# Optimization experiments

Measured on AMD Instinct MI355X. Metric: run time of the kernel, lower is better.

## Reference

```python
import jax, jax.numpy as jnp
import numpy as np

B, L, D, F = 1, 4096, 4096, 11008
# (start, end, side): side 0 = vision expert, side 1 = language expert.
# Mirrors merge_section_size over alternating contiguous vision/language token ranges.
SEGMENTS = [(0, 1024, 0), (1024, 2048, 1), (2048, 3072, 0), (3072, 4096, 1)]


def setup_inputs() -> dict:
    key = jax.random.key(0)
    ks = jax.random.split(key, 7)
    s = 0.02  # weight init scale
    hidden_states = jax.random.normal(ks[0], (B, L, D), jnp.float32)
    tt = np.zeros((B, L), np.int32)
    for a, b, side in SEGMENTS:
        tt[:, a:b] = side
    token_type_ids = jnp.asarray(tt)
    lg_w = jax.random.normal(ks[1], (D, F), jnp.float32) * s
    lu_w = jax.random.normal(ks[2], (D, F), jnp.float32) * s
    ld_w = jax.random.normal(ks[3], (F, D), jnp.float32) * s
    vg_w = jax.random.normal(ks[4], (D, F), jnp.float32) * s
    vu_w = jax.random.normal(ks[5], (D, F), jnp.float32) * s
    vd_w = jax.random.normal(ks[6], (F, D), jnp.float32) * s
    return {
        'hidden_states': hidden_states,
        'token_type_ids': token_type_ids,
        'lg_w': lg_w, 'lu_w': lu_w, 'ld_w': ld_w,
        'vg_w': vg_w, 'vu_w': vu_w, 'vd_w': vd_w,
    }


def _swiglu_mlp(x, gw, uw, dw):
    # x: [B, T, D] -> [B, T, D]; down(silu(gate(x)) * up(x))
    h = jax.nn.silu(jnp.einsum('btd,df->btf', x, gw)) * jnp.einsum('btd,df->btf', x, uw)
    return jnp.einsum('btf,fd->btd', h, dw)


def reference(hidden_states, token_type_ids, lg_w, lu_w, ld_w, vg_w, vu_w, vd_w):
    # Split-dispatch over static contiguous segments, then concat along seq dim.
    outs = []
    for a, b, side in SEGMENTS:
        seg = hidden_states[:, a:b, :]
        if side == 1:
            outs.append(_swiglu_mlp(seg, lg_w, lu_w, ld_w))
        else:
            outs.append(_swiglu_mlp(seg, vg_w, vu_w, vd_w))
    return jnp.concatenate(outs, axis=1)
```

## Files before the change

### kernel.cpp

```cpp
#include <hip/hip_runtime.h>
#include <math.h>

typedef unsigned short u16;
typedef short s16x8 __attribute__((ext_vector_type(8)));
typedef float f32x16 __attribute__((ext_vector_type(16)));

#define GLOAD16(gp, lp)                                                        \
  __builtin_amdgcn_global_load_lds(                                            \
      (const __attribute__((address_space(1))) void*)(gp),                     \
      (__attribute__((address_space(3))) void*)(lp), 16, 0, 0)

__device__ __forceinline__ u16 f2bf(float f) {
  union { float f; unsigned u; } v; v.f = f;
  unsigned r = v.u + 0x7fffu + ((v.u >> 16) & 1u);
  return (u16)(r >> 16);
}

__global__ __launch_bounds__(256) void cvt_x_kernel(const float* __restrict__ in,
                                                    u16* __restrict__ out) {
  size_t i = ((size_t)blockIdx.x * 256 + threadIdx.x) * 8;
  float4 a = *(const float4*)(in + i);
  float4 b = *(const float4*)(in + i + 4);
  s16x8 v;
  v[0] = (short)f2bf(a.x); v[1] = (short)f2bf(a.y);
  v[2] = (short)f2bf(a.z); v[3] = (short)f2bf(a.w);
  v[4] = (short)f2bf(b.x); v[5] = (short)f2bf(b.y);
  v[6] = (short)f2bf(b.z); v[7] = (short)f2bf(b.w);
  *(s16x8*)(out + i) = v;
}

__global__ __launch_bounds__(256) void transpose_cvt_kernel(
    const float* __restrict__ in0, const float* __restrict__ in1,
    const float* __restrict__ in2, const float* __restrict__ in3,
    const float* __restrict__ in4, const float* __restrict__ in5,
    u16* __restrict__ o01, u16* __restrict__ o23,
    u16* __restrict__ o4, u16* __restrict__ o5) {
  __shared__ float s[64 * 65];
  const int mat = blockIdx.y;
  const float* in; u16* out;
  switch (mat) {
    case 0: in = in0; out = o01; break;
    case 1: in = in1; out = o01; break;
    case 2: in = in2; out = o23; break;
    case 3: in = in3; out = o23; break;
    case 4: in = in4; out = o4; break;
    default: in = in5; out = o5; break;
  }
  const int R = (mat < 4) ? 4096 : 11008;
  const int C = (mat < 4) ? 11008 : 4096;
  const int nTc = C >> 6;
  const int tr = blockIdx.x / nTc, tc = blockIdx.x - tr * nTc;
  const int r0 = tr << 6, c0 = tc << 6;
  const int t = threadIdx.x;
#pragma unroll
  for (int p = 0; p < 4; ++p) {
    const int lr = p * 16 + (t >> 4);
    const int lc = (t & 15) * 4;
    float4 v = *(const float4*)(in + (size_t)(r0 + lr) * C + (c0 + lc));
    float* sp = &s[lr * 65 + lc];
    sp[0] = v.x; sp[1] = v.y; sp[2] = v.z; sp[3] = v.w;
  }
  __syncthreads();
#pragma unroll
  for (int q = 0; q < 2; ++q) {
    const int oc = q * 32 + (t >> 3);
    const int orr = (t & 7) * 8;
    s16x8 v;
#pragma unroll
    for (int i = 0; i < 8; ++i) v[i] = (short)f2bf(s[(orr + i) * 65 + oc]);
    const int f = c0 + oc;
    size_t orow;
    if (mat < 4) orow = (size_t)((f >> 7) << 8) + ((mat & 1) << 7) + (f & 127);
    else         orow = (size_t)f;
    *(s16x8*)(out + orow * R + (r0 + orr)) = v;
  }
}

#define SBAR() __builtin_amdgcn_s_barrier()
#define LGKM0() asm volatile("s_waitcnt lgkmcnt(0)")
#define VMCNT6() asm volatile("s_waitcnt vmcnt(6)")
#define VMCNT0() asm volatile("s_waitcnt vmcnt(0)")

#define LDA(d, mh)                                                             \
  do {                                                                         \
    _Pragma("unroll") for (int fj = 0; fj < 2; ++fj)                           \
        _Pragma("unroll") for (int ks = 0; ks < 4; ++ks)                       \
        af[fj][ks] = *(const s16x8*)(ldsA + (d) * 32768 + (mh) * 16384 +       \
                                     arow + fj * 4096 + cx[ks]);               \
  } while (0)
#define LDB(d, nh)                                                             \
  do {                                                                         \
    _Pragma("unroll") for (int ks = 0; ks < 4; ++ks)                           \
        bf[nh][ks] = *(const s16x8*)(ldsB + (d) * 32768 + (nh) * 16384 +       \
                                     brow + cx[ks]);                           \
  } while (0)
#define MFMA8(mh, nh)                                                          \
  do {                                                                         \
    __builtin_amdgcn_s_setprio(1);                                             \
    _Pragma("unroll") for (int fj = 0; fj < 2; ++fj)                           \
        _Pragma("unroll") for (int ks = 0; ks < 4; ++ks)                       \
        acc[mh][fj][nh] = __builtin_amdgcn_mfma_f32_32x32x16_bf16(             \
            af[fj][ks], bf[nh][ks], acc[mh][fj][nh], 0, 0, 0);                 \
    __builtin_amdgcn_s_setprio(0);                                             \
  } while (0)

#define GEMM_PIPE3(FKv, HOOK)                                                  \
  do {                                                                         \
    STG_A(0, 0, 0); STG_B(0, 0, 0); STG_B(0, 1, 0); STG_A(0, 1, 0);            \
    STG_A(1, 0, 1); STG_B(1, 0, 1); STG_B(1, 1, 1);                            \
    VMCNT6(); SBAR();                                                          \
    for (int T = 0; T < (FKv)-2; ++T) {                                        \
      const int d = T & 1, nd = d ^ 1;                                         \
      LDA(d, 0); LDB(d, 0);                                                    \
      STG_A(nd, 1, T + 1);                                                     \
      LGKM0(); MFMA8(0, 0); SBAR();                                            \
      LDB(d, 1);                                                               \
      STG_A(d, 0, T + 2); STG_B(d, 0, T + 2);                                  \
      LGKM0(); MFMA8(0, 1); SBAR();                                            \
      LDA(d, 1);                                                               \
      STG_B(d, 1, T + 2);                                                      \
      LGKM0(); MFMA8(1, 1); MFMA8(1, 0);                                       \
      VMCNT6(); SBAR();                                                        \
      HOOK;                                                                    \
    }                                                                          \
    LDA(0, 0); LDB(0, 0);                                                      \
    STG_A(1, 1, (FKv)-1);                                                      \
    LGKM0(); MFMA8(0, 0); SBAR();                                              \
    LDB(0, 1);                                                                 \
    LGKM0(); MFMA8(0, 1); SBAR();                                              \
    LDA(0, 1);                                                                 \
    LGKM0(); MFMA8(1, 1); MFMA8(1, 0);                                         \
    VMCNT0(); SBAR();                                                          \
    LDA(1, 0); LDB(1, 0);                                                      \
    LGKM0(); MFMA8(0, 0); SBAR();                                              \
    LDB(1, 1);                                                                 \
    LGKM0(); MFMA8(0, 1); SBAR();                                              \
    LDA(1, 1);                                                                 \
    LGKM0(); MFMA8(1, 1); MFMA8(1, 0);                                         \
  } while (0)

#define ZERO_ACC()                                                             \
  do {                                                                         \
    _Pragma("unroll") for (int a = 0; a < 2; ++a)                              \
        _Pragma("unroll") for (int b = 0; b < 2; ++b)                          \
        _Pragma("unroll") for (int c2 = 0; c2 < 2; ++c2)                       \
        _Pragma("unroll") for (int r = 0; r < 16; ++r) acc[a][b][c2][r] = 0.f; \
  } while (0)

__global__ __launch_bounds__(512, 1) void gemm_gateup_persist(
    const u16* __restrict__ A, const u16* __restrict__ GUl,
    const u16* __restrict__ GUv, const int* __restrict__ tt,
    u16* __restrict__ H) {
  __shared__ u16 sA[2][2][128][64];
  __shared__ u16 sB[2][2][128][64];

  const int bid = blockIdx.x;
  const int c = ((bid >> 7) << 3) | (bid & 7);
  const int mT = (bid >> 3) & 15;
  const int ntiles = (c < 6) ? 6 : 5;
  const int FK = ntiles * 64;

  const int t = threadIdx.x;
  const int lane = t & 63;
  const int l31 = lane & 31;
  const int kg = lane >> 5;
  const int wn = (t >> 6) & 3;
  const int wm = (t >> 8) & 1;

  const int side = tt[mT << 8];
  const u16* GU = side ? GUl : GUv;

  const int rowq = t >> 3;
  const int gsw = ((t & 7) ^ (rowq & 7) ^ ((rowq >> 3) & 3)) << 4;
  const char* srcA = (const char*)A + (size_t)(mT * 256 + rowq) * 8192 + gsw;
  const char* srcB0 = (const char*)GU + ((size_t)(c * 256) + rowq) * 8192 + gsw;
  char* ldsA = (char*)&sA[0][0][0][0];
  char* ldsB = (char*)&sB[0][0][0][0];
  const int woff = (t & 448) << 4;

#define STG_A(d, h, q)                                                         \
  do {                                                                         \
    const char* _pa = srcA + ((q)&63) * 128;                                   \
    GLOAD16(_pa + (size_t)((h)*128) * 8192,                                    \
            ldsA + (d)*32768 + (h)*16384 + woff);                              \
    GLOAD16(_pa + (size_t)((h)*128 + 64) * 8192,                               \
            ldsA + (d)*32768 + (h)*16384 + 8192 + woff);                       \
  } while (0)
#define STG_B(d, h, q)                                                         \
  do {                                                                         \
    const char* _pb = srcB0 + (size_t)((q) >> 6) * 33554432 +                  \
                      (size_t)((h)*128) * 8192 + ((q)&63) * 128;               \
    GLOAD16(_pb, ldsB + (d)*32768 + (h)*16384 + woff);                         \
    GLOAD16(_pb + (size_t)64 * 8192,                                           \
            ldsB + (d)*32768 + (h)*16384 + 8192 + woff);                       \
  } while (0)

  const int arow = (wm * 64 + l31) * 128;
  const int brow = (wn * 32 + l31) * 128;
  int cx[4];
#pragma unroll
  for (int ks = 0; ks < 4; ++ks)
    cx[ks] = ((2 * ks + kg) ^ (l31 & 7) ^ ((l31 >> 3) & 3)) << 4;

  s16x8 af[2][4], bf[2][4];
  f32x16 acc[2][2][2];
  ZERO_ACC();

#define GU_EPI(nTv)                                                            \
  do {                                                                         \
    const int _nT = (nTv);                                                     \
    const int f = _nT * 128 + wn * 32 + l31;                                   \
    _Pragma("unroll") for (int mh = 0; mh < 2; ++mh)                           \
        _Pragma("unroll") for (int fj = 0; fj < 2; ++fj) {                     \
      const int rowbase = mT * 256 + mh * 128 + wm * 64 + fj * 32 + 4 * kg;    \
      _Pragma("unroll") for (int r = 0; r < 16; ++r) {                         \
        const int row = rowbase + (r & 3) + 8 * (r >> 2);                      \
        const float gv = acc[mh][fj][0][r];                                    \
        const float uv = acc[mh][fj][1][r];                                    \
        const float hv = gv / (1.f + __expf(-gv)) * uv;                        \
        H[(size_t)row * 11008 + f] = f2bf(hv);                                 \
      }                                                                        \
    }                                                                          \
  } while (0)

  GEMM_PIPE3(FK, if ((T & 63) == 63) { GU_EPI(c + 16 * (T >> 6)); ZERO_ACC(); });
  GU_EPI(c + 16 * (ntiles - 1));
#undef STG_A
#undef STG_B
#undef GU_EPI
}

__global__ __launch_bounds__(512, 1) void gemm_down(
    const u16* __restrict__ Hm, const u16* __restrict__ Dl,
    const u16* __restrict__ Dv, const int* __restrict__ tt,
    float* __restrict__ O) {
  constexpr int KB = 22016;
  __shared__ u16 sA[2][2][128][64];
  __shared__ u16 sB[2][2][128][64];

  const int bid = blockIdx.x;
  const int wg = (bid & 7) * 32 + (bid >> 3);
  const int mT = wg & 15;
  const int nT = wg >> 4;

  const int t = threadIdx.x;
  const int lane = t & 63;
  const int l31 = lane & 31;
  const int kg = lane >> 5;
  const int wn = (t >> 6) & 3;
  const int wm = (t >> 8) & 1;

  const int side = tt[mT << 8];
  const u16* B = side ? Dl : Dv;

  const int rowq = t >> 3;
  const int gsw = ((t & 7) ^ (rowq & 7) ^ ((rowq >> 3) & 3)) << 4;
  const char* srcA = (const char*)Hm + (size_t)(mT * 256 + rowq) * KB + gsw;
  const char* srcB = (const char*)B + (size_t)(nT * 256 + rowq) * KB + gsw;
  char* ldsA = (char*)&sA[0][0][0][0];
  char* ldsB = (char*)&sB[0][0][0][0];
  const int woff = (t & 448) << 4;

#define STG_A(d, h, q)                                                         \
  do {                                                                         \
    GLOAD16(srcA + (size_t)((h)*128) * KB + (size_t)(q)*128,                   \
            ldsA + (d)*32768 + (h)*16384 + woff);                              \
    GLOAD16(srcA + (size_t)((h)*128 + 64) * KB + (size_t)(q)*128,              \
            ldsA + (d)*32768 + (h)*16384 + 8192 + woff);                       \
  } while (0)
#define STG_B(d, h, q)                                                         \
  do {                                                                         \
    GLOAD16(srcB + (size_t)((h)*128) * KB + (size_t)(q)*128,                   \
            ldsB + (d)*32768 + (h)*16384 + woff);                              \
    GLOAD16(srcB + (size_t)((h)*128 + 64) * KB + (size_t)(q)*128,              \
            ldsB + (d)*32768 + (h)*16384 + 8192 + woff);                       \
  } while (0)

  const int arow = (wm * 64 + l31) * 128;
  const int brow = (wn * 32 + l31) * 128;
  int cx[4];
#pragma unroll
  for (int ks = 0; ks < 4; ++ks)
    cx[ks] = ((2 * ks + kg) ^ (l31 & 7) ^ ((l31 >> 3) & 3)) << 4;

  s16x8 af[2][4], bf[2][4];
  f32x16 acc[2][2][2];
  ZERO_ACC();

  GEMM_PIPE3(172, ;);

#pragma unroll
  for (int mh = 0; mh < 2; ++mh)
#pragma unroll
    for (int fj = 0; fj < 2; ++fj) {
      const int rowbase = mT * 256 + mh * 128 + wm * 64 + fj * 32 + 4 * kg;
#pragma unroll
      for (int nh = 0; nh < 2; ++nh) {
        const int col = nT * 256 + nh * 128 + wn * 32 + l31;
#pragma unroll
        for (int r = 0; r < 16; ++r) {
          const int row = rowbase + (r & 3) + 8 * (r >> 2);
          O[(size_t)row * 4096 + col] = acc[mh][fj][nh][r];
        }
      }
    }
#undef STG_A
#undef STG_B
}

extern "C" void kernel_launch(void* const* d_in, const int* in_sizes, int n_in,
                              void* d_out, int out_size, void* d_ws, size_t ws_size,
                              hipStream_t stream) {
  (void)in_sizes; (void)n_in; (void)out_size; (void)ws_size;
  const float* x  = (const float*)d_in[0];
  const int*   tt = (const int*)d_in[1];
  const float* lg = (const float*)d_in[2];
  const float* lu = (const float*)d_in[3];
  const float* ld = (const float*)d_in[4];
  const float* vg = (const float*)d_in[5];
  const float* vu = (const float*)d_in[6];
  const float* vd = (const float*)d_in[7];

  u16* ws  = (u16*)d_ws;
  u16* xbf = ws;
  u16* GUl = xbf + 16777216;
  u16* GUv = GUl + 90177536;
  u16* ldT = GUv + 90177536;
  u16* vdT = ldT + 45088768;
  u16* hbuf = vdT + 45088768;

  cvt_x_kernel<<<dim3(8192), dim3(256), 0, stream>>>(x, xbf);
  transpose_cvt_kernel<<<dim3(11008, 6), dim3(256), 0, stream>>>(
      lg, lu, vg, vu, ld, vd, GUl, GUv, ldT, vdT);
  gemm_gateup_persist<<<dim3(256), dim3(512), 0, stream>>>(
      xbf, GUl, GUv, tt, hbuf);
  gemm_down<<<dim3(256), dim3(512), 0, stream>>>(hbuf, ldT, vdT, tt, (float*)d_out);
}
```

Baseline: 1.412 ms.

## Restructure GEMM main loop into an 8-phase barrier-interleaved pipeline

Replaces the 3-phase per-tile GEMM loop with a loop unrolled over two K-tiles. Each tile is split into four MFMA phases, each bracketed by barriers so that LDS reads, global-to-LDS staging and MFMA work interleave more finely across waves. Global stores are spread across the phases and the hook condition is adjusted for the step of two. The extra barriers add synchronisation overhead, and the change relies on FK being even for correct tail handling.

```diff
diff --git a/kernel.cpp b/kernel.cpp
--- a/kernel.cpp
+++ b/kernel.cpp
@@ -78,6 +78,7 @@
 
 #define SBAR() __builtin_amdgcn_s_barrier()
 #define LGKM0() asm volatile("s_waitcnt lgkmcnt(0)")
+#define LGKM8() asm volatile("s_waitcnt lgkmcnt(8)")
 #define VMCNT6() asm volatile("s_waitcnt vmcnt(6)")
 #define VMCNT0() asm volatile("s_waitcnt vmcnt(0)")
 
@@ -104,39 +105,58 @@
     __builtin_amdgcn_s_setprio(0);                                             \
   } while (0)
 
-#define GEMM_PIPE3(FKv, HOOK)                                                  \
+#define GEMM_PIPE8(FKv, HOOK)                                                  \
   do {                                                                         \
     STG_A(0, 0, 0); STG_B(0, 0, 0); STG_B(0, 1, 0); STG_A(0, 1, 0);            \
     STG_A(1, 0, 1); STG_B(1, 0, 1); STG_B(1, 1, 1);                            \
     VMCNT6(); SBAR();                                                          \
-    for (int T = 0; T < (FKv)-2; ++T) {                                        \
-      const int d = T & 1, nd = d ^ 1;                                         \
-      LDA(d, 0); LDB(d, 0);                                                    \
-      STG_A(nd, 1, T + 1);                                                     \
-      LGKM0(); MFMA8(0, 0); SBAR();                                            \
-      LDB(d, 1);                                                               \
-      STG_A(d, 0, T + 2); STG_B(d, 0, T + 2);                                  \
-      LGKM0(); MFMA8(0, 1); SBAR();                                            \
-      LDA(d, 1);                                                               \
-      STG_B(d, 1, T + 2);                                                      \
-      LGKM0(); MFMA8(1, 1); MFMA8(1, 0);                                       \
-      VMCNT6(); SBAR();                                                        \
+    for (int T = 0; T < (FKv)-2; T += 2) {                                     \
+      LDA(0, 0); LDB(0, 0);                                                    \
+      STG_A(1, 1, T + 1);                                                      \
+      LGKM8();                                                                 \
+      SBAR(); LGKM0(); MFMA8(0, 0); SBAR();                                    \
+      LDB(0, 1);                                                               \
+      STG_A(0, 0, T + 2);                                                      \
+      SBAR(); LGKM0(); MFMA8(0, 1); SBAR();                                    \
+      LDA(0, 1);                                                               \
+      STG_B(0, 0, T + 2);                                                      \
+      SBAR(); LGKM0(); MFMA8(1, 1); SBAR();                                    \
+      STG_B(0, 1, T + 2);                                                      \
+      VMCNT6();                                                                \
+      SBAR(); MFMA8(1, 0); SBAR();                                             \
+      LDA(1, 0); LDB(1, 0);                                                    \
+      STG_A(0, 1, T + 2);                                                      \
+      LGKM8();                                                                 \
+      SBAR(); LGKM0(); MFMA8(0, 0); SBAR();                                    \
+      LDB(1, 1);                                                               \
+      STG_A(1, 0, T + 3);                                                      \
+      SBAR(); LGKM0(); MFMA8(0, 1); SBAR();                                    \
+      LDA(1, 1);                                                               \
+      STG_B(1, 0, T + 3);                                                      \
+      SBAR(); LGKM0(); MFMA8(1, 1); SBAR();                                    \
+      STG_B(1, 1, T + 3);                                                      \
+      VMCNT6();                                                                \
+      SBAR(); MFMA8(1, 0); SBAR();                                             \
       HOOK;                                                                    \
     }                                                                          \
     LDA(0, 0); LDB(0, 0);                                                      \
     STG_A(1, 1, (FKv)-1);                                                      \
-    LGKM0(); MFMA8(0, 0); SBAR();                                              \
+    LGKM8();                                                                   \
+    SBAR(); LGKM0(); MFMA8(0, 0); SBAR();                                      \
     LDB(0, 1);                                                                 \
-    LGKM0(); MFMA8(0, 1); SBAR();                                              \
+    SBAR(); LGKM0(); MFMA8(0, 1); SBAR();                                      \
     LDA(0, 1);                                                                 \
-    LGKM0(); MFMA8(1, 1); MFMA8(1, 0);                                         \
-    VMCNT0(); SBAR();                                                          \
+    SBAR(); LGKM0(); MFMA8(1, 1); SBAR();                                      \
+    VMCNT0();                                                                  \
+    SBAR(); MFMA8(1, 0); SBAR();                                               \
     LDA(1, 0); LDB(1, 0);                                                      \
-    LGKM0(); MFMA8(0, 0); SBAR();                                              \
+    LGKM8();                                                                   \
+    SBAR(); LGKM0(); MFMA8(0, 0); SBAR();                                      \
     LDB(1, 1);                                                                 \
-    LGKM0(); MFMA8(0, 1); SBAR();                                              \
+    SBAR(); LGKM0(); MFMA8(0, 1); SBAR();                                      \
     LDA(1, 1);                                                                 \
-    LGKM0(); MFMA8(1, 1); MFMA8(1, 0);                                         \
+    SBAR(); LGKM0(); MFMA8(1, 1); SBAR();                                      \
+    MFMA8(1, 0);                                                               \
   } while (0)
 
 #define ZERO_ACC()                                                             \
@@ -223,7 +243,7 @@
     }                                                                          \
   } while (0)
 
-  GEMM_PIPE3(FK, if ((T & 63) == 63) { GU_EPI(c + 16 * (T >> 6)); ZERO_ACC(); });
+  GEMM_PIPE8(FK, if ((T & 63) == 62) { GU_EPI(c + 16 * (T >> 6)); ZERO_ACC(); });
   GU_EPI(c + 16 * (ntiles - 1));
 #undef STG_A
 #undef STG_B
@@ -287,7 +307,7 @@
   f32x16 acc[2][2][2];
   ZERO_ACC();
 
-  GEMM_PIPE3(172, ;);
+  GEMM_PIPE8(172, ;);
 
 #pragma unroll
   for (int mh = 0; mh < 2; ++mh)
```

New measurement: 1.424 ms. Within noise of the previous version (+0.9%).
